# Kernel optimization log

Measured on AMD Instinct MI355X. Metric: run time of the kernel, lower is better.

The kernel has to match this reference:

```python
import jax, jax.numpy as jnp
import numpy as np

K = 512          # patch size
H = 16           # heads
C = 768          # dim
ROPE_BASE = 100.0
COUNTS = [8000, 8300, 7800, 8668]


def _build_pad_unpad(counts, k):
    # faithful numpy replica of EfficientAttentionV2.get_padding_and_inverse
    counts = np.asarray(counts, dtype=np.int64)
    cpad = np.where(counts > k, ((counts + k - 1) // k) * k, counts)
    off = np.concatenate([[0], np.cumsum(counts)])
    offp = np.concatenate([[0], np.cumsum(cpad)])
    pad = np.arange(offp[-1])
    unpad = np.arange(off[-1])
    for i in range(len(counts)):
        unpad[off[i]:off[i + 1]] += offp[i] - off[i]
        if counts[i] != cpad[i]:
            s = offp[i + 1] - k + counts[i] % k
            pad[s:offp[i + 1]] = pad[s - k:offp[i + 1] - k]
        pad[offp[i]:offp[i + 1]] -= offp[i] - off[i]
    return pad, unpad


def setup_inputs() -> dict:
    key = jax.random.key(0)
    ks = jax.random.split(key, 6)
    N = int(np.sum(COUNTS))
    pad, unpad = _build_pad_unpad(COUNTS, K)
    rng = np.random.default_rng(0)
    perm = rng.permutation(N)                 # serialized_order stand-in
    inv_perm = np.argsort(perm)               # serialized_inverse
    order = perm[pad].astype(np.int32)        # [N_pad]
    inverse = unpad[inv_perm].astype(np.int32)  # [N]
    grid = rng.integers(0, 1024, size=(N, 3))
    pos = grid[order].astype(np.int32)        # [N_pad, 3], gathered grid coords
    s = 0.02
    return {
        "x": jax.random.normal(ks[0], (N, C), jnp.float32),
        "w_qkv": jax.random.normal(ks[1], (C, 3 * C), jnp.float32) * s,
        "b_qkv": jnp.zeros((3 * C,), jnp.float32),
        "w_proj": jax.random.normal(ks[2], (C, C), jnp.float32) * s,
        "b_proj": jnp.zeros((C,), jnp.float32),
        "order": jnp.asarray(order),
        "inverse": jnp.asarray(inverse),
        "pos": jnp.asarray(pos),
    }


def _rope1d(tok, pos1d):
    # tok: [P, K, H, d], pos1d: [P, K]
    d = tok.shape[-1]
    inv_freq = 1.0 / (ROPE_BASE ** (jnp.arange(0, d, 2, dtype=jnp.float32) / d))
    fr = pos1d[..., None].astype(jnp.float32) * inv_freq      # [P, K, d/2]
    fr = jnp.concatenate([fr, fr], axis=-1)[:, :, None, :]    # [P, K, 1, d]
    x1, x2 = jnp.split(tok, 2, axis=-1)
    rot = jnp.concatenate([-x2, x1], axis=-1)
    return tok * jnp.cos(fr) + rot * jnp.sin(fr)


def _rope3d(tok, pos):
    # tok: [P, K, H, D]; pos: [P, K, 3]; split head dim into 3 axis chunks
    parts = jnp.split(tok, 3, axis=-1)
    return jnp.concatenate(
        [_rope1d(parts[i], pos[..., i]) for i in range(3)], axis=-1)


def reference(x, w_qkv, b_qkv, w_proj, b_proj, order, inverse, pos):
    D = C // H
    scale = D ** -0.5
    qkv = x @ w_qkv + b_qkv                     # [N, 3C]
    qkv = qkv[order]                            # [N_pad, 3C] patch gather
    qkv = qkv.reshape(-1, K, 3, H, D)           # [P, K, 3, H, D]
    q, k, v = qkv[:, :, 0], qkv[:, :, 1], qkv[:, :, 2]  # [P, K, H, D]
    ppos = pos.reshape(-1, K, 3)
    q = _rope3d(q, ppos)
    k = _rope3d(k, ppos)
    attn = jnp.einsum("pkhd,pmhd->phkm", q, k) * scale
    attn = jax.nn.softmax(attn, axis=-1)
    feat = jnp.einsum("phkm,pmhd->pkhd", attn, v).reshape(-1, C)  # [N_pad, C]
    feat = feat[inverse]                        # [N, C] scatter-back
    return feat @ w_proj + b_proj
```

## Files before the change

### kernel.cpp

```cpp
#include <hip/hip_runtime.h>
#include <hip/hip_bf16.h>
#include <stdint.h>

typedef short short8 __attribute__((ext_vector_type(8)));
typedef short short4v __attribute__((ext_vector_type(4)));
typedef float f32x4 __attribute__((ext_vector_type(4)));
typedef float f32x16 __attribute__((ext_vector_type(16)));

#define AS1C(p) ((const __attribute__((address_space(1))) unsigned int*)(p))
#define AS3(p)  ((__attribute__((address_space(3))) unsigned int*)(p))

__device__ __forceinline__ short f2bf(float f) {
  union { float f; unsigned u; } v; v.f = f;
  unsigned r = v.u + 0x7FFFu + ((v.u >> 16) & 1u);
  return (short)(r >> 16);
}

__global__ void k_cast_bf16(const float* __restrict__ src, short* __restrict__ dst, int n8) {
  const int i = blockIdx.x * 256 + threadIdx.x;
  if (i >= n8) return;
  const float4* s = (const float4*)src + (size_t)i * 2;
  const float4 a = s[0], b = s[1];
  short8 o;
  o[0] = f2bf(a.x); o[1] = f2bf(a.y); o[2] = f2bf(a.z); o[3] = f2bf(a.w);
  o[4] = f2bf(b.x); o[5] = f2bf(b.y); o[6] = f2bf(b.z); o[7] = f2bf(b.w);
  ((short8*)dst)[i] = o;
}

__global__ void k_transpose_cast(const float* __restrict__ src, short* __restrict__ dst,
                                 int R, int C) {
  __shared__ float t[32][33];
  const int tx = threadIdx.x & 31, ty = threadIdx.x >> 5;
  const int c0 = blockIdx.x * 32, r0 = blockIdx.y * 32;
#pragma unroll
  for (int j = 0; j < 4; ++j)
    t[ty + j * 8][tx] = src[(size_t)(r0 + ty + j * 8) * C + c0 + tx];
  __syncthreads();
#pragma unroll
  for (int j = 0; j < 4; ++j)
    dst[(size_t)(c0 + ty + j * 8) * R + r0 + tx] = f2bf(t[tx][ty + j * 8]);
}

__global__ __launch_bounds__(256, 2)
void k_gemm1(const short* __restrict__ x16, const short* __restrict__ wt,
             const float* __restrict__ bqkv, const int* __restrict__ order,
             const int* __restrict__ pos,
             short* __restrict__ Qp, short* __restrict__ Kp, short* __restrict__ VpT) {
  __shared__ short sA[128 * 64];
  __shared__ short sB[128 * 64];
  __shared__ int sOrd[128];

  const int tid = threadIdx.x;
  const int lane = tid & 63;
  const int wv = tid >> 6;
  const int wm = wv >> 1, wn = wv & 1;
  const int tm = blockIdx.x * 128;
  const int tn = blockIdx.y * 128;

  if (tid < 128) sOrd[tid] = order[tm + tid];
  __syncthreads();

  const char* srcA[4];
  const char* srcB[4];
  {
    const int rr = tid >> 3, ck = tid & 7;
    const int sc = (ck ^ (rr & 7)) * 16;
#pragma unroll
    for (int is = 0; is < 4; ++is) {
      srcA[is] = (const char*)(x16 + (size_t)sOrd[is * 32 + rr] * 768) + sc;
      srcB[is] = (const char*)(wt + (size_t)(tn + is * 32 + rr) * 768) + sc;
    }
  }

  f32x4 acc[4][4] = {};
  const int ldsw = wv << 10;

  for (int kk = 0; kk < 12; ++kk) {
    const int kb = kk << 7;
#pragma unroll
    for (int is = 0; is < 4; ++is)
      __builtin_amdgcn_global_load_lds(AS1C(srcA[is] + kb), AS3((char*)sA + is * 4096 + ldsw), 16, 0, 0);
#pragma unroll
    for (int is = 0; is < 4; ++is)
      __builtin_amdgcn_global_load_lds(AS1C(srcB[is] + kb), AS3((char*)sB + is * 4096 + ldsw), 16, 0, 0);
    __syncthreads();

#pragma unroll
    for (int kbl = 0; kbl < 2; ++kbl) {
      const int ko = kbl * 64 + ((lane >> 4) << 4);
      short8 af[4], bf[4];
#pragma unroll
      for (int mi = 0; mi < 4; ++mi) {
        int row = wm * 64 + mi * 16 + (lane & 15);
        af[mi] = *(const short8*)((const char*)sA + row * 128 + (ko ^ ((row & 7) << 4)));
      }
#pragma unroll
      for (int ni = 0; ni < 4; ++ni) {
        int row = wn * 64 + ni * 16 + (lane & 15);
        bf[ni] = *(const short8*)((const char*)sB + row * 128 + (ko ^ ((row & 7) << 4)));
      }
#pragma unroll
      for (int mi = 0; mi < 4; ++mi)
#pragma unroll
        for (int ni = 0; ni < 4; ++ni)
          acc[mi][ni] = __builtin_amdgcn_mfma_f32_16x16x32_bf16(af[mi], bf[ni], acc[mi][ni], 0, 0, 0);
    }
    __syncthreads();
  }

  const int which = tn / 768;
  if (which == 2) {
#pragma unroll
    for (int ni = 0; ni < 4; ++ni) {
      const int col = tn + wn * 64 + ni * 16 + (lane & 15);
      const int hcol = col - 1536;
      const int h = hcol / 48;
      const int dd = hcol % 48;
      const float bq = bqkv[col];
#pragma unroll
      for (int mi = 0; mi < 4; ++mi) {
        const int m0 = tm + wm * 64 + mi * 16 + ((lane >> 4) << 2);
        const int p = m0 >> 9, q0 = m0 & 511;
        short4v vv;
#pragma unroll
        for (int r = 0; r < 4; ++r) vv[r] = f2bf(acc[mi][ni][r] + bq);
        *(short4v*)(VpT + ((size_t)(p * 16 + h) * 48 + dd) * 512 + q0) = vv;
      }
    }
  } else {
    const float invf = exp2f(-(float)(lane & 7) * 0.830482023721840f);
#pragma unroll
    for (int ni = 0; ni < 4; ++ni) {
      const int col = tn + wn * 64 + ni * 16 + (lane & 15);
      const int hcol = col - which * 768;
      const int h = hcol / 48;
      const int dd = hcol % 48;
      const int part = dd >> 4;
      const float bq = bqkv[col];
#pragma unroll
      for (int mi = 0; mi < 4; ++mi) {
        const int m0 = tm + wm * 64 + mi * 16 + ((lane >> 4) << 2);
#pragma unroll
        for (int r = 0; r < 4; ++r) {
          const int m = m0 + r;
          float val = acc[mi][ni][r] + bq;
          const int pv = pos[m * 3 + part];
          float s, c;
          __sincosf((float)pv * invf, &s, &c);
          const float partner = __shfl_xor(val, 8);
          val = val * c + ((lane & 8) ? partner : -partner) * s;
          const int p = m >> 9, q = m & 511;
          const size_t ro = (size_t)(p * 16 + h) * 512 + q;
          if (which == 0) Qp[ro * 48 + dd] = f2bf(val);
          else            Kp[(ro << 6) + dd] = f2bf(val);
        }
      }
    }
  }
}

__global__ __launch_bounds__(256, 2)
void k_attn(const short* __restrict__ Qp, const short* __restrict__ Kp,
            const short* __restrict__ VpT, short* __restrict__ featp) {
  __shared__ short sK[2][64 * 64];
  __shared__ short sV[2][64 * 64];

  const int tid = threadIdx.x;
  const int lane = tid & 63;
  const int wv = tid >> 6;
  const int l31 = lane & 31;
  const int hi = lane >> 5;
  const int bid = blockIdx.x;
  const int ph = bid >> 1;
  const int half = bid & 1;
  const int p = ph >> 4, h = ph & 15;

  ((float2*)((char*)sV[0] + 6144))[tid] = make_float2(0.f, 0.f);
  ((float2*)((char*)sV[1] + 6144))[tid] = make_float2(0.f, 0.f);

  short8 qf[2][3];
  {
    const short* Qb = Qp + ((size_t)ph * 512 + half * 256 + wv * 64) * 48;
#pragma unroll
    for (int qt = 0; qt < 2; ++qt)
#pragma unroll
      for (int dk = 0; dk < 3; ++dk)
        qf[qt][dk] = *(const short8*)(Qb + (qt * 32 + l31) * 48 + dk * 16 + hi * 8);
  }

  const char* Kb = (const char*)Kp + (size_t)ph * 65536;
  const char* Vb = (const char*)VpT + (size_t)ph * 49152;
  const int ldsw = wv << 10;

  auto stage = [&](int b, int ms) {
#pragma unroll
    for (int c = 0; c < 2; ++c) {
      const int o2 = c * 4096 + tid * 16;
      const int sw = o2 ^ ((o2 >> 3) & 0x70);
      __builtin_amdgcn_global_load_lds(AS1C(Kb + ms * 8192 + sw),
                                       AS3((char*)sK[b] + c * 4096 + ldsw), 16, 0, 0);
    }
    {
      const int o2 = tid * 16;
      const int d = o2 >> 7;
      const int inrow = (o2 & 127) ^ ((o2 >> 3) & 0x70);
      __builtin_amdgcn_global_load_lds(AS1C(Vb + (size_t)d * 1024 + ms * 128 + inrow),
                                       AS3((char*)sV[b] + ldsw), 16, 0, 0);
    }
    if (tid < 128) {
      const int o2 = 4096 + tid * 16;
      const int d = o2 >> 7;
      const int inrow = (o2 & 127) ^ ((o2 >> 3) & 0x70);
      __builtin_amdgcn_global_load_lds(AS1C(Vb + (size_t)d * 1024 + ms * 128 + inrow),
                                       AS3((char*)sV[b] + 4096 + ldsw), 16, 0, 0);
    }
  };

  stage(0, 0);
  asm volatile("s_waitcnt vmcnt(0)" ::: "memory");
  __syncthreads();

  f32x16 O[2][2] = {};
  float lr[2] = {0.f, 0.f};
  const float K2 = 0.14433756729740644f * 1.4426950408889634f;
  const float MB = 8.0f * K2;

  for (int ms = 0; ms < 8; ++ms) {
    const int bb = ms & 1;
    if (ms < 7) stage(bb ^ 1, ms + 1);

    const char* kb = (const char*)sK[bb];
    const char* vb = (const char*)sV[bb];

    f32x16 st[2][2];
    {
      short8 kf[2][3];
#pragma unroll
      for (int mt = 0; mt < 2; ++mt) {
        const int row = mt * 32 + l31;
        const int swr = (row & 7) << 4;
#pragma unroll
        for (int dk = 0; dk < 3; ++dk) {
          const int ob = (dk * 16 + hi * 8) * 2;
          kf[mt][dk] = *(const short8*)(kb + row * 128 + (ob ^ swr));
        }
      }
      __builtin_amdgcn_s_setprio(1);
#pragma unroll
      for (int mt = 0; mt < 2; ++mt)
#pragma unroll
        for (int qt = 0; qt < 2; ++qt) {
          f32x16 a = {};
#pragma unroll
          for (int dk = 0; dk < 3; ++dk)
            a = __builtin_amdgcn_mfma_f32_32x32x16_bf16(kf[mt][dk], qf[qt][dk], a, 0, 0, 0);
          st[mt][qt] = a;
        }
      __builtin_amdgcn_s_setprio(0);
    }

    unsigned pk[2][2][8];
#pragma unroll
    for (int qt = 0; qt < 2; ++qt) {
      float ps0 = 0.f, ps1 = 0.f;
#pragma unroll
      for (int mt = 0; mt < 2; ++mt) {
#pragma unroll
        for (int pr = 0; pr < 8; ++pr) {
          float p0 = __builtin_amdgcn_exp2f(st[mt][qt][pr * 2]     * K2 - MB);
          float p1 = __builtin_amdgcn_exp2f(st[mt][qt][pr * 2 + 1] * K2 - MB);
          ps0 += p0; ps1 += p1;
          __hip_bfloat162 bb2 = __float22bfloat162_rn(make_float2(p0, p1));
          unsigned w; __builtin_memcpy(&w, &bb2, 4);
          pk[mt][qt][pr] = w;
        }
      }
      lr[qt] += ps0 + ps1;
    }

    short8 vf[2][4];
#pragma unroll
    for (int dt = 0; dt < 2; ++dt) {
      const int d = dt * 32 + l31;
      const int swr = (d & 7) << 4;
#pragma unroll
      for (int ks = 0; ks < 4; ++ks) {
        const int ob = (ks * 16 + hi * 8) * 2;
        vf[dt][ks] = *(const short8*)(vb + d * 128 + (ob ^ swr));
      }
    }
#pragma unroll
    for (int qt = 0; qt < 2; ++qt) {
#pragma unroll
      for (int ks = 0; ks < 4; ++ks) {
        const int mt = ks >> 1;
        const int b0 = (ks & 1) * 4;
        const unsigned X0 = pk[mt][qt][b0 + 0];
        const unsigned X1 = pk[mt][qt][b0 + 1];
        const unsigned Y0 = pk[mt][qt][b0 + 2];
        const unsigned Y1 = pk[mt][qt][b0 + 3];
        const unsigned tX0 = __shfl_xor(X0, 32);
        const unsigned tX1 = __shfl_xor(X1, 32);
        const unsigned tY0 = __shfl_xor(Y0, 32);
        const unsigned tY1 = __shfl_xor(Y1, 32);
        union { unsigned u[4]; short8 v; } aw;
        aw.u[0] = hi ? tY0 : X0;
        aw.u[1] = hi ? tY1 : X1;
        aw.u[2] = hi ? Y0 : tX0;
        aw.u[3] = hi ? Y1 : tX1;
        __builtin_amdgcn_s_setprio(1);
#pragma unroll
        for (int dt = 0; dt < 2; ++dt)
          O[qt][dt] = __builtin_amdgcn_mfma_f32_32x32x16_bf16(aw.v, vf[dt][ks], O[qt][dt], 0, 0, 0);
        __builtin_amdgcn_s_setprio(0);
      }
    }

    if (ms < 7) {
      asm volatile("s_waitcnt vmcnt(0)" ::: "memory");
      __syncthreads();
    }
  }

#pragma unroll
  for (int qt = 0; qt < 2; ++qt) {
    float l = lr[qt] + __shfl_xor(lr[qt], 32);
    const float il = 1.0f / l;
#pragma unroll
    for (int r = 0; r < 16; ++r) {
      const int crow = (r & 3) + ((r >> 2) << 3) + (hi << 2);
      const float ilr = __shfl(il, crow);
      const int qg = half * 256 + wv * 64 + qt * 32 + crow;
      const size_t base = ((size_t)(p * 512 + qg)) * 768 + h * 48;
      featp[base + l31] = f2bf(O[qt][0][r] * ilr);
      if (l31 < 16) featp[base + 32 + l31] = f2bf(O[qt][1][r] * ilr);
    }
  }
}

__global__ __launch_bounds__(256, 2)
void k_gemm2(const short* __restrict__ featp, const short* __restrict__ wt,
             const float* __restrict__ bproj, const int* __restrict__ inverse,
             float* __restrict__ out) {
  __shared__ short sA[128 * 64];
  __shared__ short sB[128 * 64];
  __shared__ int sInv[128];

  const int tid = threadIdx.x;
  const int lane = tid & 63;
  const int wv = tid >> 6;
  const int wm = wv >> 1, wn = wv & 1;
  const int tm = blockIdx.x * 128;
  const int tn = blockIdx.y * 128;

  if (tid < 128) sInv[tid] = inverse[tm + tid];
  __syncthreads();

  const char* srcA[4];
  const char* srcB[4];
  {
    const int rr = tid >> 3, ck = tid & 7;
    const int sc = (ck ^ (rr & 7)) * 16;
#pragma unroll
    for (int is = 0; is < 4; ++is) {
      srcA[is] = (const char*)(featp + (size_t)sInv[is * 32 + rr] * 768) + sc;
      srcB[is] = (const char*)(wt + (size_t)(tn + is * 32 + rr) * 768) + sc;
    }
  }

  f32x4 acc[4][4] = {};
  const int ldsw = wv << 10;

  for (int kk = 0; kk < 12; ++kk) {
    const int kb = kk << 7;
#pragma unroll
    for (int is = 0; is < 4; ++is)
      __builtin_amdgcn_global_load_lds(AS1C(srcA[is] + kb), AS3((char*)sA + is * 4096 + ldsw), 16, 0, 0);
#pragma unroll
    for (int is = 0; is < 4; ++is)
      __builtin_amdgcn_global_load_lds(AS1C(srcB[is] + kb), AS3((char*)sB + is * 4096 + ldsw), 16, 0, 0);
    __syncthreads();

#pragma unroll
    for (int kbl = 0; kbl < 2; ++kbl) {
      const int ko = kbl * 64 + ((lane >> 4) << 4);
      short8 af[4], bf[4];
#pragma unroll
      for (int mi = 0; mi < 4; ++mi) {
        int row = wm * 64 + mi * 16 + (lane & 15);
        af[mi] = *(const short8*)((const char*)sA + row * 128 + (ko ^ ((row & 7) << 4)));
      }
#pragma unroll
      for (int ni = 0; ni < 4; ++ni) {
        int row = wn * 64 + ni * 16 + (lane & 15);
        bf[ni] = *(const short8*)((const char*)sB + row * 128 + (ko ^ ((row & 7) << 4)));
      }
#pragma unroll
      for (int mi = 0; mi < 4; ++mi)
#pragma unroll
        for (int ni = 0; ni < 4; ++ni)
          acc[mi][ni] = __builtin_amdgcn_mfma_f32_16x16x32_bf16(af[mi], bf[ni], acc[mi][ni], 0, 0, 0);
    }
    __syncthreads();
  }

#pragma unroll
  for (int ni = 0; ni < 4; ++ni) {
    const int col = tn + wn * 64 + ni * 16 + (lane & 15);
    const float bq = bproj[col];
#pragma unroll
    for (int mi = 0; mi < 4; ++mi) {
      const int m0 = tm + wm * 64 + mi * 16 + ((lane >> 4) << 2);
#pragma unroll
      for (int r = 0; r < 4; ++r)
        out[(size_t)(m0 + r) * 768 + col] = acc[mi][ni][r] + bq;
    }
  }
}

extern "C" void kernel_launch(void* const* d_in, const int* in_sizes, int n_in,
                              void* d_out, int out_size, void* d_ws, size_t ws_size,
                              hipStream_t stream) {
  (void)n_in; (void)out_size; (void)ws_size;
  const float* x      = (const float*)d_in[0];
  const float* w_qkv  = (const float*)d_in[1];
  const float* b_qkv  = (const float*)d_in[2];
  const float* w_proj = (const float*)d_in[3];
  const float* b_proj = (const float*)d_in[4];
  const int* order    = (const int*)d_in[5];
  const int* inverse  = (const int*)d_in[6];
  const int* pos      = (const int*)d_in[7];
  float* out = (float*)d_out;

  const int N = in_sizes[6];
  const int Npad = in_sizes[5];

  char* ws = (char*)d_ws;
  const size_t szTok = (size_t)Npad * 768 * 2;
  short* x16   = (short*)ws;
  short* featp = (short*)ws;
  short* wt1 = (short*)(ws + szTok);
  short* wt2 = (short*)(ws + szTok + 3538944);
  short* Qp  = (short*)(ws + szTok + 3538944 + 1179648);
  short* Kp  = (short*)(ws + szTok * 2 + 3538944 + 1179648);
  short* VpT = (short*)(ws + szTok * 2 + 3538944 + 1179648 + (size_t)Npad * 2048);

  k_cast_bf16<<<dim3((N * 768 / 8 + 255) / 256), 256, 0, stream>>>(x, x16, N * 768 / 8);
  k_transpose_cast<<<dim3(2304 / 32, 768 / 32), 256, 0, stream>>>(w_qkv, wt1, 768, 2304);
  k_transpose_cast<<<dim3(768 / 32, 768 / 32), 256, 0, stream>>>(w_proj, wt2, 768, 768);
  k_gemm1<<<dim3(Npad / 128, 18), 256, 0, stream>>>(x16, wt1, b_qkv, order, pos, Qp, Kp, VpT);
  k_attn<<<dim3((Npad / 512) * 16 * 2), 256, 0, stream>>>(Qp, Kp, VpT, featp);
  k_gemm2<<<dim3(N / 128, 6), 256, 0, stream>>>(featp, wt2, b_proj, inverse, out);
}
```

Baseline: 397.3 us.

## Enlarge QKV GEMM tile to 256x256 and double-buffer LDS loads

The QKV projection GEMM now uses 256x256 output tiles with 512 threads. Each wave computes a 128x64 sub-tile. The K loop double-buffers the A and B tiles in LDS, issuing the next slice's asynchronous global-to-LDS loads while MFMAs run on the current slice, and raises wave priority around the MFMA block. The aim is more operand reuse per LDS byte and hiding global load latency that the single-buffered loop exposed at every step. In exchange, LDS use rises to about 128KB per block, which allows only one block per CU, and the grid has far fewer blocks.

```diff
diff --git a/kernel.cpp b/kernel.cpp
--- a/kernel.cpp
+++ b/kernel.cpp
@@ -41,23 +41,24 @@
     dst[(size_t)(c0 + ty + j * 8) * R + r0 + tx] = f2bf(t[tx][ty + j * 8]);
 }
 
-__global__ __launch_bounds__(256, 2)
+__global__ __launch_bounds__(512, 2)
 void k_gemm1(const short* __restrict__ x16, const short* __restrict__ wt,
              const float* __restrict__ bqkv, const int* __restrict__ order,
              const int* __restrict__ pos,
              short* __restrict__ Qp, short* __restrict__ Kp, short* __restrict__ VpT) {
-  __shared__ short sA[128 * 64];
-  __shared__ short sB[128 * 64];
-  __shared__ int sOrd[128];
+  __shared__ short sA[2][256 * 64];
+  __shared__ short sB[2][256 * 64];
+  __shared__ int sOrd[256];
 
   const int tid = threadIdx.x;
   const int lane = tid & 63;
   const int wv = tid >> 6;
-  const int wm = wv >> 1, wn = wv & 1;
-  const int tm = blockIdx.x * 128;
-  const int tn = blockIdx.y * 128;
-
-  if (tid < 128) sOrd[tid] = order[tm + tid];
+  const int wm = wv >> 2;
+  const int wn = wv & 3;
+  const int tm = blockIdx.x * 256;
+  const int tn = blockIdx.y * 256;
+
+  if (tid < 256) sOrd[tid] = order[tm + tid];
   __syncthreads();
 
   const char* srcA[4];
@@ -67,45 +68,74 @@
     const int sc = (ck ^ (rr & 7)) * 16;
 #pragma unroll
     for (int is = 0; is < 4; ++is) {
-      srcA[is] = (const char*)(x16 + (size_t)sOrd[is * 32 + rr] * 768) + sc;
-      srcB[is] = (const char*)(wt + (size_t)(tn + is * 32 + rr) * 768) + sc;
-    }
-  }
-
-  f32x4 acc[4][4] = {};
+      srcA[is] = (const char*)(x16 + (size_t)sOrd[is * 64 + rr] * 768) + sc;
+      srcB[is] = (const char*)(wt + (size_t)(tn + is * 64 + rr) * 768) + sc;
+    }
+  }
   const int ldsw = wv << 10;
 
-  for (int kk = 0; kk < 12; ++kk) {
-    const int kb = kk << 7;
-#pragma unroll
-    for (int is = 0; is < 4; ++is)
-      __builtin_amdgcn_global_load_lds(AS1C(srcA[is] + kb), AS3((char*)sA + is * 4096 + ldsw), 16, 0, 0);
-#pragma unroll
-    for (int is = 0; is < 4; ++is)
-      __builtin_amdgcn_global_load_lds(AS1C(srcB[is] + kb), AS3((char*)sB + is * 4096 + ldsw), 16, 0, 0);
-    __syncthreads();
-
-#pragma unroll
-    for (int kbl = 0; kbl < 2; ++kbl) {
+  f32x4 acc[8][4] = {};
+
+#pragma unroll
+  for (int is = 0; is < 4; ++is)
+    __builtin_amdgcn_global_load_lds(AS1C(srcA[is]), AS3((char*)sA[0] + is * 8192 + ldsw), 16, 0, 0);
+#pragma unroll
+  for (int is = 0; is < 4; ++is)
+    __builtin_amdgcn_global_load_lds(AS1C(srcB[is]), AS3((char*)sB[0] + is * 8192 + ldsw), 16, 0, 0);
+
+  for (int t = 0; t < 12; ++t) {
+    const int cur = t & 1;
+    const char* ka = (const char*)sA[cur];
+    const char* kb = (const char*)sB[cur];
+    const int kbn = (t + 1) << 7;
+
+    short8 bf[4];
+#pragma unroll
+    for (int p = 0; p < 4; ++p) {
+      const int kbl = p >> 1;
+      const int mh = p & 1;
       const int ko = kbl * 64 + ((lane >> 4) << 4);
-      short8 af[4], bf[4];
-#pragma unroll
-      for (int mi = 0; mi < 4; ++mi) {
-        int row = wm * 64 + mi * 16 + (lane & 15);
-        af[mi] = *(const short8*)((const char*)sA + row * 128 + (ko ^ ((row & 7) << 4)));
-      }
-#pragma unroll
-      for (int ni = 0; ni < 4; ++ni) {
-        int row = wn * 64 + ni * 16 + (lane & 15);
-        bf[ni] = *(const short8*)((const char*)sB + row * 128 + (ko ^ ((row & 7) << 4)));
-      }
-#pragma unroll
-      for (int mi = 0; mi < 4; ++mi)
+
+      if (p == 0) asm volatile("s_waitcnt vmcnt(0)" ::: "memory");
+      asm volatile("s_barrier" ::: "memory");
+
+      short8 af[4];
+      if (mh == 0) {
+#pragma unroll
+        for (int ni = 0; ni < 4; ++ni) {
+          const int row = wn * 64 + ni * 16 + (lane & 15);
+          bf[ni] = *(const short8*)(kb + row * 128 + (ko ^ ((row & 7) << 4)));
+        }
+      }
+#pragma unroll
+      for (int i = 0; i < 4; ++i) {
+        const int row = wm * 128 + (mh * 4 + i) * 16 + (lane & 15);
+        af[i] = *(const short8*)(ka + row * 128 + (ko ^ ((row & 7) << 4)));
+      }
+
+      if (t < 11) {
+        if (p == 0) {
+#pragma unroll
+          for (int is = 0; is < 4; ++is)
+            __builtin_amdgcn_global_load_lds(AS1C(srcA[is] + kbn),
+                AS3((char*)sA[cur ^ 1] + is * 8192 + ldsw), 16, 0, 0);
+        } else if (p == 1) {
+#pragma unroll
+          for (int is = 0; is < 4; ++is)
+            __builtin_amdgcn_global_load_lds(AS1C(srcB[is] + kbn),
+                AS3((char*)sB[cur ^ 1] + is * 8192 + ldsw), 16, 0, 0);
+        }
+      }
+
+      __builtin_amdgcn_s_setprio(1);
+#pragma unroll
+      for (int i = 0; i < 4; ++i)
 #pragma unroll
         for (int ni = 0; ni < 4; ++ni)
-          acc[mi][ni] = __builtin_amdgcn_mfma_f32_16x16x32_bf16(af[mi], bf[ni], acc[mi][ni], 0, 0, 0);
-    }
-    __syncthreads();
+          acc[mh * 4 + i][ni] =
+              __builtin_amdgcn_mfma_f32_16x16x32_bf16(af[i], bf[ni], acc[mh * 4 + i][ni], 0, 0, 0);
+      __builtin_amdgcn_s_setprio(0);
+    }
   }
 
   const int which = tn / 768;
@@ -118,8 +148,8 @@
       const int dd = hcol % 48;
       const float bq = bqkv[col];
 #pragma unroll
-      for (int mi = 0; mi < 4; ++mi) {
-        const int m0 = tm + wm * 64 + mi * 16 + ((lane >> 4) << 2);
+      for (int mi = 0; mi < 8; ++mi) {
+        const int m0 = tm + wm * 128 + mi * 16 + ((lane >> 4) << 2);
         const int p = m0 >> 9, q0 = m0 & 511;
         short4v vv;
 #pragma unroll
@@ -138,8 +168,8 @@
       const int part = dd >> 4;
       const float bq = bqkv[col];
 #pragma unroll
-      for (int mi = 0; mi < 4; ++mi) {
-        const int m0 = tm + wm * 64 + mi * 16 + ((lane >> 4) << 2);
+      for (int mi = 0; mi < 8; ++mi) {
+        const int m0 = tm + wm * 128 + mi * 16 + ((lane >> 4) << 2);
 #pragma unroll
         for (int r = 0; r < 4; ++r) {
           const int m = m0 + r;
@@ -448,7 +478,7 @@
   k_cast_bf16<<<dim3((N * 768 / 8 + 255) / 256), 256, 0, stream>>>(x, x16, N * 768 / 8);
   k_transpose_cast<<<dim3(2304 / 32, 768 / 32), 256, 0, stream>>>(w_qkv, wt1, 768, 2304);
   k_transpose_cast<<<dim3(768 / 32, 768 / 32), 256, 0, stream>>>(w_proj, wt2, 768, 768);
-  k_gemm1<<<dim3(Npad / 128, 18), 256, 0, stream>>>(x16, wt1, b_qkv, order, pos, Qp, Kp, VpT);
+  k_gemm1<<<dim3(Npad / 256, 9), 512, 0, stream>>>(x16, wt1, b_qkv, order, pos, Qp, Kp, VpT);
   k_attn<<<dim3((Npad / 512) * 16 * 2), 256, 0, stream>>>(Qp, Kp, VpT, featp);
   k_gemm2<<<dim3(N / 128, 6), 256, 0, stream>>>(featp, wt2, b_proj, inverse, out);
 }
```

Measured after the change: 417.2 us. +5.0%, slower.

## Triple-buffer attention K/V staging and precompute RoPE sin/cos table

Applied to the files above, without the earlier changes.

The attention kernel moves from double to triple buffering of K/V tiles in LDS, prefetching two tiles ahead. It waits with counted vmcnt and issues one barrier per iteration instead of a full drain plus sync at the end of each step. Separately, a small kernel precomputes a cos/sin lookup table over positions 0..1023 and 8 frequencies, and the QK GEMM epilogue reads it instead of calling sincos. The changes raise LDS use per block, which may lower occupancy, and the table assumes positions stay below 1024.

```diff
diff --git a/kernel.cpp b/kernel.cpp
--- a/kernel.cpp
+++ b/kernel.cpp
@@ -27,6 +27,16 @@
   ((short8*)dst)[i] = o;
 }
 
+__global__ void k_sintab(float2* __restrict__ tbl) {
+  const int i = blockIdx.x * 256 + threadIdx.x;
+  const int f = i & 7;
+  const int pv = i >> 3;
+  const float invf = exp2f(-(float)f * 0.830482023721840f);
+  float s, c;
+  __sincosf((float)pv * invf, &s, &c);
+  tbl[i] = make_float2(c, s);
+}
+
 __global__ void k_transpose_cast(const float* __restrict__ src, short* __restrict__ dst,
                                  int R, int C) {
   __shared__ float t[32][33];
@@ -44,7 +54,7 @@
 __global__ __launch_bounds__(256, 2)
 void k_gemm1(const short* __restrict__ x16, const short* __restrict__ wt,
              const float* __restrict__ bqkv, const int* __restrict__ order,
-             const int* __restrict__ pos,
+             const int* __restrict__ pos, const float2* __restrict__ stab,
              short* __restrict__ Qp, short* __restrict__ Kp, short* __restrict__ VpT) {
   __shared__ short sA[128 * 64];
   __shared__ short sB[128 * 64];
@@ -128,7 +138,6 @@
       }
     }
   } else {
-    const float invf = exp2f(-(float)(lane & 7) * 0.830482023721840f);
 #pragma unroll
     for (int ni = 0; ni < 4; ++ni) {
       const int col = tn + wn * 64 + ni * 16 + (lane & 15);
@@ -145,10 +154,9 @@
           const int m = m0 + r;
           float val = acc[mi][ni][r] + bq;
           const int pv = pos[m * 3 + part];
-          float s, c;
-          __sincosf((float)pv * invf, &s, &c);
+          const float2 cs = stab[(pv << 3) + (lane & 7)];
           const float partner = __shfl_xor(val, 8);
-          val = val * c + ((lane & 8) ? partner : -partner) * s;
+          val = val * cs.x + ((lane & 8) ? partner : -partner) * cs.y;
           const int p = m >> 9, q = m & 511;
           const size_t ro = (size_t)(p * 16 + h) * 512 + q;
           if (which == 0) Qp[ro * 48 + dd] = f2bf(val);
@@ -162,8 +170,8 @@
 __global__ __launch_bounds__(256, 2)
 void k_attn(const short* __restrict__ Qp, const short* __restrict__ Kp,
             const short* __restrict__ VpT, short* __restrict__ featp) {
-  __shared__ short sK[2][64 * 64];
-  __shared__ short sV[2][64 * 64];
+  __shared__ short sK[3][64 * 64];
+  __shared__ short sV[3][64 * 64];
 
   const int tid = threadIdx.x;
   const int lane = tid & 63;
@@ -175,8 +183,9 @@
   const int half = bid & 1;
   const int p = ph >> 4, h = ph & 15;
 
-  ((float2*)((char*)sV[0] + 6144))[tid] = make_float2(0.f, 0.f);
-  ((float2*)((char*)sV[1] + 6144))[tid] = make_float2(0.f, 0.f);
+#pragma unroll
+  for (int b = 0; b < 3; ++b)
+    ((float2*)((char*)sV[b] + 6144))[tid] = make_float2(0.f, 0.f);
 
   short8 qf[2][3];
   {
@@ -217,20 +226,27 @@
   };
 
   stage(0, 0);
-  asm volatile("s_waitcnt vmcnt(0)" ::: "memory");
-  __syncthreads();
+  stage(1, 1);
 
   f32x16 O[2][2] = {};
   float lr[2] = {0.f, 0.f};
   const float K2 = 0.14433756729740644f * 1.4426950408889634f;
   const float MB = 8.0f * K2;
 
+#pragma unroll 1
   for (int ms = 0; ms < 8; ++ms) {
-    const int bb = ms & 1;
-    if (ms < 7) stage(bb ^ 1, ms + 1);
-
-    const char* kb = (const char*)sK[bb];
-    const char* vb = (const char*)sV[bb];
+    if (ms < 7) {
+      if (tid < 128) asm volatile("s_waitcnt vmcnt(4)" ::: "memory");
+      else           asm volatile("s_waitcnt vmcnt(3)" ::: "memory");
+    } else {
+      asm volatile("s_waitcnt vmcnt(0)" ::: "memory");
+    }
+    if (ms == 0) asm volatile("s_waitcnt lgkmcnt(0)" ::: "memory");
+    __builtin_amdgcn_s_barrier();
+
+    if (ms < 6) stage((ms + 2) % 3, ms + 2);
+    const char* kb = (const char*)sK + (ms % 3) * 8192;
+    const char* vb = (const char*)sV + (ms % 3) * 8192;
 
     f32x16 st[2][2];
     {
@@ -315,11 +331,6 @@
         __builtin_amdgcn_s_setprio(0);
       }
     }
-
-    if (ms < 7) {
-      asm volatile("s_waitcnt vmcnt(0)" ::: "memory");
-      __syncthreads();
-    }
   }
 
 #pragma unroll
@@ -444,11 +455,13 @@
   short* Qp  = (short*)(ws + szTok + 3538944 + 1179648);
   short* Kp  = (short*)(ws + szTok * 2 + 3538944 + 1179648);
   short* VpT = (short*)(ws + szTok * 2 + 3538944 + 1179648 + (size_t)Npad * 2048);
+  float2* stab = (float2*)(ws + szTok * 3 + 3538944 + 1179648 + (size_t)Npad * 2048);
 
   k_cast_bf16<<<dim3((N * 768 / 8 + 255) / 256), 256, 0, stream>>>(x, x16, N * 768 / 8);
+  k_sintab<<<dim3(32), 256, 0, stream>>>(stab);
   k_transpose_cast<<<dim3(2304 / 32, 768 / 32), 256, 0, stream>>>(w_qkv, wt1, 768, 2304);
   k_transpose_cast<<<dim3(768 / 32, 768 / 32), 256, 0, stream>>>(w_proj, wt2, 768, 768);
-  k_gemm1<<<dim3(Npad / 128, 18), 256, 0, stream>>>(x16, wt1, b_qkv, order, pos, Qp, Kp, VpT);
+  k_gemm1<<<dim3(Npad / 128, 18), 256, 0, stream>>>(x16, wt1, b_qkv, order, pos, stab, Qp, Kp, VpT);
   k_attn<<<dim3((Npad / 512) * 16 * 2), 256, 0, stream>>>(Qp, Kp, VpT, featp);
   k_gemm2<<<dim3(N / 128, 6), 256, 0, stream>>>(featp, wt2, b_proj, inverse, out);
 }
```

New measurement: 415.1 us. +4.5%, slower.
